# Optimization experiments

Hardware: AMD Instinct MI355X
Metric: run time of the kernel (lower is better)

## Reference

```python
import jax, jax.numpy as jnp
import numpy as np


def setup_inputs() -> dict:
    key = jax.random.key(0)
    ks = jax.random.split(key, 11)
    B, E, R, D = 2048, 20000, 500, 256
    inp = {
        "h": jax.random.uniform(ks[0], (B, E), dtype=jnp.float32),
        "t": jax.random.uniform(ks[1], (B, E), dtype=jnp.float32),
        "r": jax.random.uniform(ks[2], (B, R), dtype=jnp.float32),
        "W_er": jax.random.normal(ks[3], (D, E), dtype=jnp.float32) * 0.02,
        "W_ei": jax.random.normal(ks[4], (D, E), dtype=jnp.float32) * 0.02,
        "W_ej": jax.random.normal(ks[5], (D, E), dtype=jnp.float32) * 0.02,
        "W_ek": jax.random.normal(ks[6], (D, E), dtype=jnp.float32) * 0.02,
        "W_rr": jax.random.normal(ks[7], (D, R), dtype=jnp.float32) * 0.02,
        "W_ri": jax.random.normal(ks[8], (D, R), dtype=jnp.float32) * 0.02,
        "W_rj": jax.random.normal(ks[9], (D, R), dtype=jnp.float32) * 0.02,
        "W_rk": jax.random.normal(ks[10], (D, R), dtype=jnp.float32) * 0.02,
    }
    return inp


def reference(h, t, r, W_er, W_ei, W_ej, W_ek, W_rr, W_ri, W_rj, W_rk):
    # entity / relation projections (nn.Linear, no bias): x @ W^T -> [B, D]
    H_r, H_i, H_j, H_k = h @ W_er.T, h @ W_ei.T, h @ W_ej.T, h @ W_ek.T
    T_r, T_i, T_j, T_k = t @ W_er.T, t @ W_ei.T, t @ W_ej.T, t @ W_ek.T
    R_r, R_i, R_j, R_k = r @ W_rr.T, r @ W_ri.T, r @ W_rj.T, r @ W_rk.T

    # hypercomplex norm per row: sqrt(|R_r|^2 + |R_i|^2 + |R_j|^2 + |R_k|^2) -> [B,1]
    norm = jnp.sqrt(
        jnp.sum(R_r * R_r + R_i * R_i + R_j * R_j + R_k * R_k, axis=1, keepdims=True)
    )
    R_r, R_i, R_j, R_k = norm * R_r, norm * R_i, norm * R_j, norm * R_k

    # Hamilton product H (x) R
    Q_r = H_r * R_r - H_i * R_i - H_j * R_j - H_k * R_k
    Q_i = H_r * R_i + H_i * R_r + H_j * R_k - H_k * R_j
    Q_j = H_r * R_j - H_i * R_k + H_j * R_r + H_k * R_i
    Q_k = H_r * R_k + H_i * R_j - H_j * R_i + H_k * R_r

    # diag(Q @ T^T) == rowwise dot sum(Q*T, axis=1) -- O(B*d) form of the anti-pattern
    score = jnp.sum(Q_r * T_r + Q_i * T_i + Q_j * T_j + Q_k * T_k, axis=1, keepdims=True)
    return jax.nn.sigmoid(score)
```

## Files before the change

kernel.cpp:

```cpp
#include <hip/hip_runtime.h>


using bf16x8 = __attribute__((ext_vector_type(8))) short;
using f32x4  = __attribute__((ext_vector_type(4))) float;
using f32x16 = __attribute__((ext_vector_type(16))) float;

#define DEVINL static __device__ __forceinline__

DEVINL void split2(float x0, float x1, unsigned& h, unsigned& l) {
  unsigned u0 = __float_as_uint(x0), u1 = __float_as_uint(x1);
  unsigned h0 = u0 & 0xFFFF0000u, h1 = u1 & 0xFFFF0000u;
  h = (u0 >> 16) | h1;
  float r0 = x0 - __uint_as_float(h0);
  float r1 = x1 - __uint_as_float(h1);
  l = (__float_as_uint(r0) >> 16) | (__float_as_uint(r1) & 0xFFFF0000u);
}

DEVINL void gload16(const void* g, void* l) {
  __builtin_amdgcn_global_load_lds(
      (const __attribute__((address_space(1))) unsigned*)g,
      (__attribute__((address_space(3))) unsigned*)l, 16, 0, 0);
}

__global__ void convert_img(const float* __restrict__ src0,
                            const float* __restrict__ src1, int rows0,
                            int srcK, char* __restrict__ dst, int ktiles,
                            int rtile)
{
  const int kt = blockIdx.x, rt = blockIdx.y;
  const int m  = threadIdx.x;
  const int row = rt * rtile + m;
  const float* srow = (row < rows0) ? (src0 + (size_t)row * srcK)
                                    : (src1 + (size_t)(row - rows0) * srcK);
  const size_t tileB = (size_t)rtile * 128;
  const int plane = rtile * 64;
  char* base = dst + ((size_t)rt * ktiles + kt) * tileB
             + (m >> 5) * 2048 + (m & 31) * 16;
#pragma unroll
  for (int oct = 0; oct < 4; ++oct) {
    int k0 = kt * 32 + oct * 8;
    float x[8];
    if (k0 + 8 <= srcK) {
      float4 v0 = *(const float4*)(srow + k0);
      float4 v1 = *(const float4*)(srow + k0 + 4);
      x[0] = v0.x; x[1] = v0.y; x[2] = v0.z; x[3] = v0.w;
      x[4] = v1.x; x[5] = v1.y; x[6] = v1.z; x[7] = v1.w;
    } else {
#pragma unroll
      for (int j = 0; j < 8; ++j) x[j] = (k0 + j < srcK) ? srow[k0 + j] : 0.f;
    }
    unsigned hh[4], ll[4];
    split2(x[0], x[1], hh[0], ll[0]);
    split2(x[2], x[3], hh[1], ll[1]);
    split2(x[4], x[5], hh[2], ll[2]);
    split2(x[6], x[7], hh[3], ll[3]);
    int off = (oct >> 1) * 1024 + (oct & 1) * 512;
    *(uint4*)(base + off)         = make_uint4(hh[0], hh[1], hh[2], hh[3]);
    *(uint4*)(base + plane + off) = make_uint4(ll[0], ll[1], ll[2], ll[3]);
  }
}

__global__ __launch_bounds__(512, 1) void gemm_img(
    const char* __restrict__ Aimg, const char* __restrict__ Bimg, int ktiles,
    float* __restrict__ C, int MT, int NT, int KS, int swz)
{
  __shared__ __align__(16) char smem[131072];
  const int bid = blockIdx.x;

  int mt, nt, ks;
  if (swz) {
    int x = bid & 7, w = bid >> 3;
    nt = w & 3;
    int g = x + (w >> 2) * 8;
    mt = g & 15; ks = g >> 4;
  } else {
    nt = bid % NT; int q = bid / NT; mt = q % MT; ks = q / MT;
  }

  const int kt0 = (ktiles * ks) / KS;
  const int kt1 = (ktiles * (ks + 1)) / KS;

  const char* Ab = Aimg + ((size_t)mt * ktiles + kt0) * 32768;
  const char* Bb = Bimg + ((size_t)nt * ktiles + kt0) * 32768;

  const int wid = threadIdx.x >> 6, lane = threadIdx.x & 63;
  const int wr = wid >> 2, wc = wid & 3;

  f32x16 acc[4][2];
#pragma unroll
  for (int mb = 0; mb < 4; ++mb)
#pragma unroll
    for (int nb = 0; nb < 2; ++nb)
#pragma unroll
      for (int e = 0; e < 16; ++e) acc[mb][nb][e] = 0.f;

  {
    const char* As = Ab + wid * 4096 + lane * 16;
    const char* Bs = Bb + wid * 4096 + lane * 16;
#pragma unroll
    for (int i = 0; i < 4; ++i) gload16(As + i * 1024, smem + wid * 4096 + i * 1024);
#pragma unroll
    for (int i = 0; i < 4; ++i) gload16(Bs + i * 1024, smem + 32768 + wid * 4096 + i * 1024);
  }
  asm volatile("s_waitcnt vmcnt(0)" ::: "memory");
  __builtin_amdgcn_s_barrier();

  for (int kt = kt0; kt < kt1; ++kt) {
    char* bufc = smem + (size_t)((kt - kt0) & 1) * 65536;
    char* bufn = smem + (size_t)(((kt - kt0) & 1) ^ 1) * 65536;
    const bool nx = (kt + 1 < kt1);

    if (nx) {
      const char* As = Ab + (size_t)(kt + 1 - kt0) * 32768 + wid * 4096 + lane * 16;
      const char* Bs = Bb + (size_t)(kt + 1 - kt0) * 32768 + wid * 4096 + lane * 16;
#pragma unroll
      for (int i = 0; i < 4; ++i) gload16(As + i * 1024, bufn + wid * 4096 + i * 1024);
#pragma unroll
      for (int i = 0; i < 4; ++i) gload16(Bs + i * 1024, bufn + 32768 + wid * 4096 + i * 1024);
    }

    bf16x8 bh[2][2], bl[2][2];
#pragma unroll
    for (int nb = 0; nb < 2; ++nb)
#pragma unroll
      for (int s = 0; s < 2; ++s) {
        const char* p = bufc + 32768 + (wc * 2 + nb) * 2048 + s * 1024 + lane * 16;
        bh[nb][s] = *(const bf16x8*)p;
        bl[nb][s] = *(const bf16x8*)(p + 16384);
      }

    bf16x8 pah[2][2], pal[2][2];
#pragma unroll
    for (int s = 0; s < 2; ++s) {
      const char* p = bufc + (wr * 4 + 0) * 2048 + s * 1024 + lane * 16;
      pah[0][s] = *(const bf16x8*)p;
      pal[0][s] = *(const bf16x8*)(p + 16384);
    }

#pragma unroll
    for (int mb = 0; mb < 4; ++mb) {
      const int cur = mb & 1, nxt = cur ^ 1;
      if (mb < 3) {
#pragma unroll
        for (int s = 0; s < 2; ++s) {
          const char* p = bufc + (wr * 4 + mb + 1) * 2048 + s * 1024 + lane * 16;
          pah[nxt][s] = *(const bf16x8*)p;
          pal[nxt][s] = *(const bf16x8*)(p + 16384);
        }
      }
      __builtin_amdgcn_sched_barrier(0);
      __builtin_amdgcn_s_setprio(1);
#pragma unroll
      for (int nb = 0; nb < 2; ++nb)
#pragma unroll
        for (int s = 0; s < 2; ++s) {
          f32x16* a = &acc[mb][nb];
          *a = __builtin_amdgcn_mfma_f32_32x32x16_bf16(pah[cur][s], bh[nb][s], *a, 0, 0, 0);
          *a = __builtin_amdgcn_mfma_f32_32x32x16_bf16(pal[cur][s], bh[nb][s], *a, 0, 0, 0);
          *a = __builtin_amdgcn_mfma_f32_32x32x16_bf16(pah[cur][s], bl[nb][s], *a, 0, 0, 0);
        }
      __builtin_amdgcn_s_setprio(0);
      __builtin_amdgcn_sched_barrier(0);
    }

    asm volatile("s_waitcnt vmcnt(0)" ::: "memory");
    __builtin_amdgcn_s_barrier();
  }

  float* Cb = C + (size_t)ks * (size_t)(MT * 256) * 1024;
  const long rowbase = (long)mt * 256 + wr * 128 + 4 * (lane >> 5);
  const long colbase = (long)nt * 256 + wc * 64 + (lane & 31);
#pragma unroll
  for (int mb = 0; mb < 4; ++mb)
#pragma unroll
    for (int nb = 0; nb < 2; ++nb)
#pragma unroll
      for (int reg = 0; reg < 16; ++reg) {
        long row = rowbase + mb * 32 + (reg & 3) + 8 * (reg >> 2);
        long col = colbase + nb * 32;
        Cb[(size_t)row * 1024 + col] = acc[mb][nb][reg];
      }
}

__global__ void convert_b16(const float* __restrict__ src, int srcK,
                            char* __restrict__ dst)
{
  const int tile = blockIdx.x;
  const int wrow = threadIdx.x;
  char* base = dst + (size_t)tile * 32768;
  const float* srow = src + (size_t)wrow * srcK;
#pragma unroll
  for (int kc8 = 0; kc8 < 4; ++kc8) {
    int k0 = tile * 32 + kc8 * 8;
    float x[8];
    if (k0 + 8 <= srcK) {
      float4 v0 = *(const float4*)(srow + k0);
      float4 v1 = *(const float4*)(srow + k0 + 4);
      x[0] = v0.x; x[1] = v0.y; x[2] = v0.z; x[3] = v0.w;
      x[4] = v1.x; x[5] = v1.y; x[6] = v1.z; x[7] = v1.w;
    } else {
#pragma unroll
      for (int j = 0; j < 8; ++j) x[j] = (k0 + j < srcK) ? srow[k0 + j] : 0.f;
    }
    unsigned hh[4], ll[4];
    split2(x[0], x[1], hh[0], ll[0]);
    split2(x[2], x[3], hh[1], ll[1]);
    split2(x[4], x[5], hh[2], ll[2]);
    split2(x[6], x[7], hh[3], ll[3]);
    int lchunk = (wrow & 15) + kc8 * 16;
    int n16 = wrow >> 4;
    *(uint4*)(base + (size_t)n16 * 1024 + lchunk * 16)         = make_uint4(hh[0], hh[1], hh[2], hh[3]);
    *(uint4*)(base + 16384 + (size_t)n16 * 1024 + lchunk * 16) = make_uint4(ll[0], ll[1], ll[2], ll[3]);
  }
}

__global__ void pad_r(const float* __restrict__ src, float* __restrict__ dst)
{
  int row = blockIdx.y;
  int k = threadIdx.x * 4;
  float4 v = make_float4(0.f, 0.f, 0.f, 0.f);
  if (k + 3 < 500) v = *(const float4*)(src + (size_t)row * 500 + k);
  *(float4*)(dst + (size_t)row * 512 + k) = v;
}

__global__ __launch_bounds__(512, 2) void gemm3p(
    const float* __restrict__ A0, const float* __restrict__ A1, int mtA0, long lda,
    const char* __restrict__ Bimg, int ktilesTot,
    float* __restrict__ C, long ldc, int MT, int NT, int KS, int swz)
{
  extern __shared__ char smemd[];
  const int tid = threadIdx.x;
  const int bid = blockIdx.x;

  int mt, nt, ks;
  if (swz) {
    int x = bid & 7, w = bid >> 3;
    nt = w & 3;
    int g = x + (w >> 2) * 8;
    mt = g & 15; ks = g >> 4;
  } else {
    nt = bid % NT; int q = bid / NT; mt = q % MT; ks = q / MT;
  }

  const int kt0 = (ktilesTot * ks) / KS;
  const int kt1 = (ktilesTot * (ks + 1)) / KS;

  const float* Ablk = (mt < mtA0) ? (A0 + (size_t)mt * 256 * lda)
                                  : (A1 + (size_t)(mt - mtA0) * 256 * lda);
  const char* Bt = Bimg + ((size_t)nt * ktilesTot + kt0) * 32768;

  const int wid = tid >> 6, lane = tid & 63;
  const int wr = wid >> 2, wc = wid & 3;
  const int l15 = lane & 15, lq = lane >> 4;

  const float* aSrc = Ablk + (size_t)(wid * 32 + (lane >> 3)) * lda
                      + (size_t)kt0 * 32 + 4 * (lane & 7);

  int awoff[4];
  {
    int kg = (lane & 7) >> 1, half = lane & 1;
#pragma unroll
    for (int i = 0; i < 4; ++i) {
      int m15 = (lane >> 3) + 8 * (i & 1);
      awoff[i] = (2 * wid + (i >> 1)) * 2048 + (((m15 ^ kg) + kg * 16) << 4) + half * 8;
    }
  }
  const int aroff = (((l15 ^ lq) + lq * 16) << 4);
  const int bbase = 32768 + (wc * 4) * 1024 + lane * 16;

  f32x4 acc[8][4];
#pragma unroll
  for (int m = 0; m < 8; ++m)
#pragma unroll
    for (int j = 0; j < 4; ++j)
#pragma unroll
      for (int e = 0; e < 4; ++e) acc[m][j][e] = 0.f;

  float4 aR[4];

#define ISSUE_A(KT)                                                            \
  {                                                                            \
    const float* p_ = aSrc + (size_t)((KT) - kt0) * 32;                        \
    _Pragma("unroll")                                                          \
    for (int i = 0; i < 4; ++i) aR[i] = *(const float4*)(p_ + (size_t)(8 * i) * lda); \
  }
#define ISSUE_B(DST, KT)                                                       \
  {                                                                            \
    const char* p_ = Bt + (size_t)((KT) - kt0) * 32768 + wid * 4096 + lane * 16; \
    _Pragma("unroll")                                                          \
    for (int i = 0; i < 4; ++i)                                                \
      gload16(p_ + i * 1024, (DST) + 32768 + wid * 4096 + i * 1024);           \
  }
#define WRITE_A(DST)                                                           \
  {                                                                            \
    _Pragma("unroll")                                                          \
    for (int i = 0; i < 4; ++i) {                                              \
      unsigned h0_, l0_, h1_, l1_;                                             \
      split2(aR[i].x, aR[i].y, h0_, l0_);                                      \
      split2(aR[i].z, aR[i].w, h1_, l1_);                                      \
      *(uint2*)((DST) + awoff[i])        = make_uint2(h0_, h1_);               \
      *(uint2*)((DST) + awoff[i] + 1024) = make_uint2(l0_, l1_);               \
    }                                                                          \
  }

  ISSUE_A(kt0);
  ISSUE_B(smemd, kt0);
  WRITE_A(smemd);
  asm volatile("s_waitcnt vmcnt(0)" ::: "memory");
  asm volatile("s_waitcnt lgkmcnt(0)" ::: "memory");
  __builtin_amdgcn_s_barrier();

  for (int kt = kt0; kt < kt1; ++kt) {
    char* bufc = smemd + (size_t)((kt - kt0) & 1) * 65536;
    char* bufn = smemd + (size_t)(((kt - kt0) & 1) ^ 1) * 65536;
    const bool nx = (kt + 1 < kt1);

    if (nx) { ISSUE_A(kt + 1); ISSUE_B(bufn, kt + 1); }

    bf16x8 bh[4], bl[4];
#pragma unroll
    for (int j = 0; j < 4; ++j) {
      bh[j] = *(const bf16x8*)(bufc + bbase + j * 1024);
      bl[j] = *(const bf16x8*)(bufc + bbase + j * 1024 + 16384);
    }

    __builtin_amdgcn_s_setprio(1);
#pragma unroll
    for (int m = 0; m < 4; ++m) {
      const char* ab = bufc + (wr * 8 + m) * 2048;
      bf16x8 ah = *(const bf16x8*)(ab + aroff);
      bf16x8 al = *(const bf16x8*)(ab + aroff + 1024);
#pragma unroll
      for (int j = 0; j < 4; ++j) {
        acc[m][j] = __builtin_amdgcn_mfma_f32_16x16x32_bf16(ah, bh[j], acc[m][j], 0, 0, 0);
        acc[m][j] = __builtin_amdgcn_mfma_f32_16x16x32_bf16(al, bh[j], acc[m][j], 0, 0, 0);
        acc[m][j] = __builtin_amdgcn_mfma_f32_16x16x32_bf16(ah, bl[j], acc[m][j], 0, 0, 0);
      }
    }
    __builtin_amdgcn_s_setprio(0);

    __builtin_amdgcn_sched_barrier(0);
    if (nx) WRITE_A(bufn);

    __builtin_amdgcn_s_setprio(1);
#pragma unroll
    for (int m = 4; m < 8; ++m) {
      const char* ab = bufc + (wr * 8 + m) * 2048;
      bf16x8 ah = *(const bf16x8*)(ab + aroff);
      bf16x8 al = *(const bf16x8*)(ab + aroff + 1024);
#pragma unroll
      for (int j = 0; j < 4; ++j) {
        acc[m][j] = __builtin_amdgcn_mfma_f32_16x16x32_bf16(ah, bh[j], acc[m][j], 0, 0, 0);
        acc[m][j] = __builtin_amdgcn_mfma_f32_16x16x32_bf16(al, bh[j], acc[m][j], 0, 0, 0);
        acc[m][j] = __builtin_amdgcn_mfma_f32_16x16x32_bf16(ah, bl[j], acc[m][j], 0, 0, 0);
      }
    }
    __builtin_amdgcn_s_setprio(0);

    asm volatile("s_waitcnt vmcnt(0)" ::: "memory");
    asm volatile("s_waitcnt lgkmcnt(0)" ::: "memory");
    __builtin_amdgcn_s_barrier();
  }
#undef ISSUE_A
#undef ISSUE_B
#undef WRITE_A

  float* Cb = C + (size_t)ks * (size_t)(MT * 256) * (size_t)ldc;
  const long rowbase = (long)mt * 256 + wr * 128 + lq * 4;
  const long colbase = (long)nt * 256 + wc * 64 + l15;
#pragma unroll
  for (int m = 0; m < 8; ++m)
#pragma unroll
    for (int j = 0; j < 4; ++j)
#pragma unroll
      for (int reg = 0; reg < 4; ++reg) {
        long row = rowbase + m * 16 + reg;
        long col = colbase + j * 16;
        Cb[(size_t)row * ldc + col] = acc[m][j][reg];
      }
}

__global__ void epilogue_kernel(const float* __restrict__ C1, const float* __restrict__ C2,
                                float* __restrict__ out, int KS)
{
  const int b = blockIdx.x;
  const int d = threadIdx.x;
  const size_t SZ = 4096ull * 1024ull;

  float Hq[4], Tq[4], Rq[4];
#pragma unroll
  for (int q = 0; q < 4; ++q) {
    float hv = 0.f, tv = 0.f;
    for (int ks = 0; ks < KS; ++ks) {
      hv += C1[ks * SZ + (size_t)b * 1024 + q * 256 + d];
      tv += C1[ks * SZ + (size_t)(b + 2048) * 1024 + q * 256 + d];
    }
    Hq[q] = hv; Tq[q] = tv;
    Rq[q] = C2[(size_t)b * 1024 + q * 256 + d];
  }
  float nn = Rq[0]*Rq[0] + Rq[1]*Rq[1] + Rq[2]*Rq[2] + Rq[3]*Rq[3];
  float Qr = Hq[0]*Rq[0] - Hq[1]*Rq[1] - Hq[2]*Rq[2] - Hq[3]*Rq[3];
  float Qi = Hq[0]*Rq[1] + Hq[1]*Rq[0] + Hq[2]*Rq[3] - Hq[3]*Rq[2];
  float Qj = Hq[0]*Rq[2] - Hq[1]*Rq[3] + Hq[2]*Rq[0] + Hq[3]*Rq[1];
  float Qk = Hq[0]*Rq[3] + Hq[1]*Rq[2] - Hq[2]*Rq[1] + Hq[3]*Rq[0];
  float ss = Qr*Tq[0] + Qi*Tq[1] + Qj*Tq[2] + Qk*Tq[3];

#pragma unroll
  for (int o = 32; o; o >>= 1) {
    ss += __shfl_xor(ss, o);
    nn += __shfl_xor(nn, o);
  }
  __shared__ float red[8];
  int lane = d & 63, w = d >> 6;
  if (lane == 0) { red[w] = ss; red[4 + w] = nn; }
  __syncthreads();
  if (d == 0) {
    float S = red[0] + red[1] + red[2] + red[3];
    float N = red[4] + red[5] + red[6] + red[7];
    float score = sqrtf(N) * S;
    out[b] = 1.f / (1.f + expf(-score));
  }
}

extern "C" void kernel_launch(void* const* d_in, const int* in_sizes, int n_in,
                              void* d_out, int out_size, void* d_ws, size_t ws_size,
                              hipStream_t stream)
{
  const float* h = (const float*)d_in[0];
  const float* t = (const float*)d_in[1];
  const float* r = (const float*)d_in[2];
  const float* We[4] = {(const float*)d_in[3], (const float*)d_in[4],
                        (const float*)d_in[5], (const float*)d_in[6]};
  const float* Wr[4] = {(const float*)d_in[7], (const float*)d_in[8],
                        (const float*)d_in[9], (const float*)d_in[10]};
  float* out = (float*)d_out;
  char* ws = (char*)d_ws;

  const size_t offA  = 0;
  const size_t offB  = 327680000;
  const size_t offWr = offB + 81920000;
  const size_t offRi = offWr + 2097152;
  const size_t offC1 = offRi + 4194304;
  const size_t C1sz  = 4096ull * 1024ull * 4ull;
  const size_t offC2 = offC1 + 4 * C1sz;
  const size_t needImg = offC2 + 8388608;

  if (ws_size >= needImg) {
    float* C1 = (float*)(ws + offC1);
    float* C2 = (float*)(ws + offC2);

    convert_img<<<dim3(625, 16), 256, 0, stream>>>(h, t, 2048, 20000, ws + offA, 625, 256);
    for (int q = 0; q < 4; ++q) {
      convert_img<<<dim3(625, 1), 256, 0, stream>>>(
          We[q], We[q], 2048, 20000, ws + offB + (size_t)q * 625 * 32768, 625, 256);
      convert_img<<<dim3(16, 1), 256, 0, stream>>>(
          Wr[q], Wr[q], 2048, 500, ws + offWr + (size_t)q * 16 * 32768, 16, 256);
    }
    convert_img<<<dim3(16, 8), 256, 0, stream>>>(r, r, 2048, 500, ws + offRi, 16, 256);

    gemm_img<<<dim3(256), 512, 0, stream>>>(
        ws + offA, ws + offB, 625, C1, 16, 4, 4, 1);
    gemm_img<<<dim3(32), 512, 0, stream>>>(
        ws + offRi, ws + offWr, 16, C2, 8, 4, 1, 0);

    epilogue_kernel<<<dim3(2048), 256, 0, stream>>>(C1, C2, out, 4);
    return;
  }

  const size_t fB  = 0;
  const size_t fWr = 81920000;
  const size_t fR  = fWr + 2097152;
  const size_t fC1 = fR + 4194304;
  const int KS = (ws_size >= fC1 + 4 * C1sz + 8388608ull) ? 4 : 2;
  const size_t fC2 = fC1 + (size_t)KS * C1sz;

  float* rpad = (float*)(ws + fR);
  float* C1   = (float*)(ws + fC1);
  float* C2   = (float*)(ws + fC2);

  for (int q = 0; q < 4; ++q) {
    convert_b16<<<dim3(625), 256, 0, stream>>>(We[q], 20000, ws + fB + (size_t)q * 625 * 32768);
    convert_b16<<<dim3(16), 256, 0, stream>>>(Wr[q], 500, ws + fWr + (size_t)q * 16 * 32768);
  }
  pad_r<<<dim3(1, 2048), 128, 0, stream>>>(r, rpad);

  gemm3p<<<dim3(16 * 4 * KS), 512, 131072, stream>>>(
      h, t, 8, 20000L, (const char*)(ws + fB), 625,
      C1, 1024L, 16, 4, KS, KS == 4 ? 1 : 0);
  gemm3p<<<dim3(32), 512, 131072, stream>>>(
      rpad, rpad, 8, 512L, (const char*)(ws + fWr), 16,
      C2, 1024L, 8, 4, 1, 0);

  epilogue_kernel<<<dim3(2048), 256, 0, stream>>>(C1, C2, out, KS);
}
```

Before: 678.8 us.

## Load A fragments directly from global into registers, stage only B in LDS

The GEMM kernel now reads each wave's A fragments straight from global memory into registers, prefetching the next tile's fragments midway through the current tile. Only B goes through LDS via global_load_lds, which halves shared memory to 64KB. The wave tiling changes from 2x4 to 4x2 so each wave owns 64 rows by 128 columns. This removes A's LDS round trip and its LDS read traffic, at the cost of more registers for the double-buffered A fragments and a partial vmcnt wait that must match the load counts exactly.

```diff
diff --git a/kernel.cpp b/kernel.cpp
--- a/kernel.cpp
+++ b/kernel.cpp
@@ -60,11 +60,11 @@
   }
 }
 
-__global__ __launch_bounds__(512, 1) void gemm_img(
+__global__ __launch_bounds__(512, 1) void gemm_ad(
     const char* __restrict__ Aimg, const char* __restrict__ Bimg, int ktiles,
     float* __restrict__ C, int MT, int NT, int KS, int swz)
 {
-  __shared__ __align__(16) char smem[131072];
+  __shared__ __align__(16) char smem[65536];
   const int bid = blockIdx.x;
 
   int mt, nt, ks;
@@ -80,100 +80,124 @@
   const int kt0 = (ktiles * ks) / KS;
   const int kt1 = (ktiles * (ks + 1)) / KS;
 
-  const char* Ab = Aimg + ((size_t)mt * ktiles + kt0) * 32768;
-  const char* Bb = Bimg + ((size_t)nt * ktiles + kt0) * 32768;
+  const char* Akt = Aimg + ((size_t)mt * ktiles + kt0) * 32768;
+  const char* Bkt = Bimg + ((size_t)nt * ktiles + kt0) * 32768;
 
   const int wid = threadIdx.x >> 6, lane = threadIdx.x & 63;
-  const int wr = wid >> 2, wc = wid & 3;
-
-  f32x16 acc[4][2];
-#pragma unroll
-  for (int mb = 0; mb < 4; ++mb)
-#pragma unroll
-    for (int nb = 0; nb < 2; ++nb)
+  const int wr = wid >> 1, wc = wid & 1;
+
+  const int abase = (wr * 2) * 2048 + lane * 16;
+  const int bbase = (wc * 4) * 2048 + lane * 16;
+  const int soff  = wid * 4096 + lane * 16;
+
+  f32x16 acc[2][4];
+#pragma unroll
+  for (int mb = 0; mb < 2; ++mb)
+#pragma unroll
+    for (int nb = 0; nb < 4; ++nb)
 #pragma unroll
       for (int e = 0; e < 16; ++e) acc[mb][nb][e] = 0.f;
 
-  {
-    const char* As = Ab + wid * 4096 + lane * 16;
-    const char* Bs = Bb + wid * 4096 + lane * 16;
-#pragma unroll
-    for (int i = 0; i < 4; ++i) gload16(As + i * 1024, smem + wid * 4096 + i * 1024);
-#pragma unroll
-    for (int i = 0; i < 4; ++i) gload16(Bs + i * 1024, smem + 32768 + wid * 4096 + i * 1024);
-  }
+  bf16x8 aA[8], aB[8];
+  bf16x8 bb[2][4];
+
+#pragma unroll
+  for (int i = 0; i < 4; ++i)
+    gload16(Bkt + soff + i * 1024, smem + soff + i * 1024);
+#pragma unroll
+  for (int mb = 0; mb < 2; ++mb)
+#pragma unroll
+    for (int s = 0; s < 2; ++s)
+#pragma unroll
+      for (int pl = 0; pl < 2; ++pl)
+        aA[mb * 4 + s * 2 + pl] =
+            *(const bf16x8*)(Akt + pl * 16384 + mb * 2048 + s * 1024 + abase);
   asm volatile("s_waitcnt vmcnt(0)" ::: "memory");
+  __builtin_amdgcn_sched_barrier(0);
   __builtin_amdgcn_s_barrier();
-
-  for (int kt = kt0; kt < kt1; ++kt) {
-    char* bufc = smem + (size_t)((kt - kt0) & 1) * 65536;
-    char* bufn = smem + (size_t)(((kt - kt0) & 1) ^ 1) * 65536;
-    const bool nx = (kt + 1 < kt1);
-
-    if (nx) {
-      const char* As = Ab + (size_t)(kt + 1 - kt0) * 32768 + wid * 4096 + lane * 16;
-      const char* Bs = Bb + (size_t)(kt + 1 - kt0) * 32768 + wid * 4096 + lane * 16;
-#pragma unroll
-      for (int i = 0; i < 4; ++i) gload16(As + i * 1024, bufn + wid * 4096 + i * 1024);
-#pragma unroll
-      for (int i = 0; i < 4; ++i) gload16(Bs + i * 1024, bufn + 32768 + wid * 4096 + i * 1024);
-    }
-
-    bf16x8 bh[2][2], bl[2][2];
-#pragma unroll
-    for (int nb = 0; nb < 2; ++nb)
-#pragma unroll
-      for (int s = 0; s < 2; ++s) {
-        const char* p = bufc + 32768 + (wc * 2 + nb) * 2048 + s * 1024 + lane * 16;
-        bh[nb][s] = *(const bf16x8*)p;
-        bl[nb][s] = *(const bf16x8*)(p + 16384);
-      }
-
-    bf16x8 pah[2][2], pal[2][2];
-#pragma unroll
-    for (int s = 0; s < 2; ++s) {
-      const char* p = bufc + (wr * 4 + 0) * 2048 + s * 1024 + lane * 16;
-      pah[0][s] = *(const bf16x8*)p;
-      pal[0][s] = *(const bf16x8*)(p + 16384);
-    }
-
-#pragma unroll
-    for (int mb = 0; mb < 4; ++mb) {
-      const int cur = mb & 1, nxt = cur ^ 1;
-      if (mb < 3) {
-#pragma unroll
-        for (int s = 0; s < 2; ++s) {
-          const char* p = bufc + (wr * 4 + mb + 1) * 2048 + s * 1024 + lane * 16;
-          pah[nxt][s] = *(const bf16x8*)p;
-          pal[nxt][s] = *(const bf16x8*)(p + 16384);
-        }
-      }
-      __builtin_amdgcn_sched_barrier(0);
-      __builtin_amdgcn_s_setprio(1);
-#pragma unroll
-      for (int nb = 0; nb < 2; ++nb)
-#pragma unroll
-        for (int s = 0; s < 2; ++s) {
-          f32x16* a = &acc[mb][nb];
-          *a = __builtin_amdgcn_mfma_f32_32x32x16_bf16(pah[cur][s], bh[nb][s], *a, 0, 0, 0);
-          *a = __builtin_amdgcn_mfma_f32_32x32x16_bf16(pal[cur][s], bh[nb][s], *a, 0, 0, 0);
-          *a = __builtin_amdgcn_mfma_f32_32x32x16_bf16(pah[cur][s], bl[nb][s], *a, 0, 0, 0);
-        }
-      __builtin_amdgcn_s_setprio(0);
-      __builtin_amdgcn_sched_barrier(0);
-    }
-
-    asm volatile("s_waitcnt vmcnt(0)" ::: "memory");
-    __builtin_amdgcn_s_barrier();
-  }
+  Akt += 32768; Bkt += 32768;
+
+#define TILE(AC, AN, BUFC, BUFN, NX)                                           \
+  {                                                                            \
+    if (NX) {                                                                  \
+      _Pragma("unroll")                                                        \
+      for (int i = 0; i < 4; ++i)                                              \
+        gload16(Bkt + soff + i * 1024, (BUFN) + soff + i * 1024);              \
+    }                                                                          \
+    __builtin_amdgcn_sched_barrier(0);    \
+    _Pragma("unroll")                                                          \
+    for (int s = 0; s < 2; ++s)                                                \
+      _Pragma("unroll")                                                        \
+      for (int pl = 0; pl < 2; ++pl)                                           \
+        bb[0][s * 2 + pl] =                                                    \
+            *(const bf16x8*)((BUFC) + pl * 16384 + s * 1024 + bbase);          \
+    _Pragma("unroll")                                                          \
+    for (int nb = 0; nb < 4; ++nb) {                                           \
+      const int cur = nb & 1, nxt = cur ^ 1;                                   \
+      if (nb < 3) {                                                            \
+        _Pragma("unroll")                                                      \
+        for (int s = 0; s < 2; ++s)                                            \
+          _Pragma("unroll")                                                    \
+          for (int pl = 0; pl < 2; ++pl)                                       \
+            bb[nxt][s * 2 + pl] = *(const bf16x8*)((BUFC) + pl * 16384 +       \
+                                  (nb + 1) * 2048 + s * 1024 + bbase);         \
+      }                                                                        \
+      __builtin_amdgcn_s_setprio(1);                                           \
+      _Pragma("unroll")                                                        \
+      for (int mb = 0; mb < 2; ++mb)                                           \
+        _Pragma("unroll")                                                      \
+        for (int s = 0; s < 2; ++s) {                                          \
+          f32x16* a = &acc[mb][nb];                                            \
+          bf16x8 ah = (AC)[mb * 4 + s * 2 + 0];                                \
+          bf16x8 al = (AC)[mb * 4 + s * 2 + 1];                                \
+          bf16x8 bhv = bb[cur][s * 2 + 0];                                     \
+          bf16x8 blv = bb[cur][s * 2 + 1];                                     \
+          *a = __builtin_amdgcn_mfma_f32_32x32x16_bf16(ah, bhv, *a, 0, 0, 0);  \
+          *a = __builtin_amdgcn_mfma_f32_32x32x16_bf16(al, bhv, *a, 0, 0, 0);  \
+          *a = __builtin_amdgcn_mfma_f32_32x32x16_bf16(ah, blv, *a, 0, 0, 0);  \
+        }                                                                      \
+      __builtin_amdgcn_s_setprio(0);                                           \
+      if (nb == 1 && (NX)) {                                                   \
+        _Pragma("unroll")                                                      \
+        for (int s = 0; s < 2; ++s)                                            \
+          _Pragma("unroll")                                                    \
+          for (int pl = 0; pl < 2; ++pl)                                       \
+            (AN)[s * 2 + pl] =                                                 \
+                *(const bf16x8*)(Akt + pl * 16384 + s * 1024 + abase);         \
+      }                                                                        \
+      if (nb == 3 && (NX)) {                                                   \
+        _Pragma("unroll")                                                      \
+        for (int s = 0; s < 2; ++s)                                            \
+          _Pragma("unroll")                                                    \
+          for (int pl = 0; pl < 2; ++pl)                                       \
+            (AN)[4 + s * 2 + pl] = *(const bf16x8*)(Akt + pl * 16384 +         \
+                                   2048 + s * 1024 + abase);                   \
+      }                                                                        \
+    }                                                                          \
+    __builtin_amdgcn_sched_barrier(0);                                         \
+    if (NX) { asm volatile("s_waitcnt vmcnt(8)" ::: "memory"); }               \
+    else    { asm volatile("s_waitcnt vmcnt(0)" ::: "memory"); }               \
+    __builtin_amdgcn_sched_barrier(0);                                         \
+    __builtin_amdgcn_s_barrier();                                              \
+    if (NX) { Akt += 32768; Bkt += 32768; }                                    \
+  }
+
+  int kt = kt0;
+  while (kt + 2 <= kt1) {
+    TILE(aA, aB, smem, smem + 32768, true);
+    TILE(aB, aA, smem + 32768, smem, (kt + 2) < kt1);
+    kt += 2;
+  }
+  if (kt < kt1) TILE(aA, aB, smem, smem + 32768, false);
+#undef TILE
 
   float* Cb = C + (size_t)ks * (size_t)(MT * 256) * 1024;
-  const long rowbase = (long)mt * 256 + wr * 128 + 4 * (lane >> 5);
-  const long colbase = (long)nt * 256 + wc * 64 + (lane & 31);
-#pragma unroll
-  for (int mb = 0; mb < 4; ++mb)
-#pragma unroll
-    for (int nb = 0; nb < 2; ++nb)
+  const long rowbase = (long)mt * 256 + wr * 64 + 4 * (lane >> 5);
+  const long colbase = (long)nt * 256 + wc * 128 + (lane & 31);
+#pragma unroll
+  for (int mb = 0; mb < 2; ++mb)
+#pragma unroll
+    for (int nb = 0; nb < 4; ++nb)
 #pragma unroll
       for (int reg = 0; reg < 16; ++reg) {
         long row = rowbase + mb * 32 + (reg & 3) + 8 * (reg >> 2);
@@ -458,9 +482,9 @@
     }
     convert_img<<<dim3(16, 8), 256, 0, stream>>>(r, r, 2048, 500, ws + offRi, 16, 256);
 
-    gemm_img<<<dim3(256), 512, 0, stream>>>(
+    gemm_ad<<<dim3(256), 512, 0, stream>>>(
         ws + offA, ws + offB, 625, C1, 16, 4, 4, 1);
-    gemm_img<<<dim3(32), 512, 0, stream>>>(
+    gemm_ad<<<dim3(32), 512, 0, stream>>>(
         ws + offRi, ws + offWr, 16, C2, 8, 4, 1, 0);
 
     epilogue_kernel<<<dim3(2048), 256, 0, stream>>>(C1, C2, out, 4);
```

Result: slower. 699.7 us (+3.1%).
